# Optimization experiments

Measured on AMD Instinct MI355X. Metric: run time of the kernel, lower is better.

## Reference

```python
import jax, jax.numpy as jnp
import numpy as np

WD = 7                      # width == height == 7 (hard-coded 6/7 constants in source)
SCALE = 0.3
NUM_CLASSES = 17
IN_FEAT = NUM_CLASSES * 10 * WD * WD  # 8330
BS = 4096
GROUPS = [("head", 2), ("arm", 2), ("upper", 2), ("lower", 2), ("foot", 1)]
KEY_IDX = {"head": [0, 1, 3, 4], "arm": [7, 8, 9, 10], "upper": [5, 6, 11, 12],
           "lower": [11, 12, 13, 14], "foot": [15, 16]}


def setup_inputs() -> dict:
    key = jax.random.key(0)
    ks = jax.random.split(key, 2 + 2 * len(GROUPS))
    inp = {
        "x": jax.random.normal(ks[0], (BS, IN_FEAT), jnp.float32),
        "keypoint": jax.random.uniform(ks[1], (BS, 17, 2), jnp.float32),
    }
    i = 2
    for name, g in GROUPS:
        inp[f"W_{name}"] = jax.random.normal(ks[i], (IN_FEAT, g * 2 * WD), jnp.float32) * 0.01
        inp[f"b_{name}"] = jax.random.normal(ks[i + 1], (g * 2 * WD,), jnp.float32) * 0.01
        i += 2
    return inp


def _gen_map(vec, kp):
    """vec: (bs, G, 2, WD) float; kp: (bs, K, 2) int32. Returns (bs, G, 1, WD, WD)."""
    v = jnp.exp(jax.nn.softmax(vec, axis=2))  # softmax over the size-2 axis, then exp
    cols = jnp.arange(WD)

    def cum(a, keep):  # masked normalize + cumsum; a: (bs,G,WD), keep: (bs,1,WD) bool
        am = jnp.where(keep, a, 0.0)
        return jnp.cumsum(am / am.sum(-1, keepdims=True), axis=-1)

    def axis_mask(a, k):  # a: (bs,G,WD), k: (bs,K) int
        lo = jnp.maximum(k.min(axis=1) - 1, 0)[:, None, None]          # zero cols < lo
        hi = jnp.minimum(k.max(axis=1) + 1, WD - 1)[:, None, None]      # zero cols >= hi
        c1 = cum(a, cols >= lo)
        c1 = jnp.where(c1 >= SCALE, c1, 0.0)
        c2 = 1.0 - cum(a, cols < hi)
        c2 = jnp.where(c2 >= SCALE, c2, 0.0)
        return c1 * c2

    xm = axis_mask(v[:, :, 0], kp[:, :, 0])   # (bs,G,WD)
    ym = axis_mask(v[:, :, 1], kp[:, :, 1])   # (bs,G,WD)
    m = ym[:, :, :, None] * xm[:, :, None, :]  # (bs,G,WD,WD): rows=y, cols=x
    # per-sample global max over (G,WD,WD); .item() in torch detaches it
    mx = jax.lax.stop_gradient(m.max(axis=(1, 2, 3), keepdims=True))
    m = m / (mx + 1e-7)
    return m[:, :, None]  # (bs, G, 1, WD, WD)


def reference(x, keypoint, W_head, b_head, W_arm, b_arm, W_upper, b_upper,
              W_lower, b_lower, W_foot, b_foot):
    bs = x.shape[0]
    kp = jnp.minimum(jnp.floor(keypoint * 7.0).astype(jnp.int32), 6)  # (bs,17,2)
    params = {"head": (W_head, b_head), "arm": (W_arm, b_arm),
              "upper": (W_upper, b_upper), "lower": (W_lower, b_lower),
              "foot": (W_foot, b_foot)}
    outs = []
    for name, _ in GROUPS:
        W, b = params[name]
        vec = (x @ W + b).reshape(bs, -1, 2, WD)            # (bs,G,2,WD)
        outs.append(_gen_map(vec, kp[:, jnp.array(KEY_IDX[name])]))
    return tuple(outs)
```

## Files before the change

### kernel.cpp

```cpp
#include <hip/hip_runtime.h>

typedef _Float16 half8 __attribute__((ext_vector_type(8)));
typedef float f32x4 __attribute__((ext_vector_type(4)));

#define WD 7
#define NPAD 128
#define KDIM 8330
#define BSZ 4096
#define SPLITK 8
#define NTILES 261
#define BM 64
#define BK 32

static constexpr size_t OFF_WT   = 0;
static constexpr size_t WT_BYTES = (size_t)NTILES * 16384;
static constexpr size_t OFF_BIAS = WT_BYTES;
static constexpr size_t OFF_PART = OFF_BIAS + 512;

static __device__ const int KIDX[5][4] = {
    {0, 1, 3, 4}, {7, 8, 9, 10}, {5, 6, 11, 12}, {11, 12, 13, 14}, {15, 16, 15, 16}};
static __device__ const unsigned long long OBASE[5] = {0ull, 401408ull, 802816ull, 1204224ull, 1605632ull};

__device__ __forceinline__ int tile0_of(int s) { return 33 * s - max(0, s - 5); }
__device__ __forceinline__ int niter_of(int s) { return (s < 5) ? 33 : 32; }

__device__ __forceinline__ unsigned pk16(_Float16 a, _Float16 b) {
  return (unsigned)__builtin_bit_cast(unsigned short, a) |
         ((unsigned)__builtin_bit_cast(unsigned short, b) << 16);
}

__device__ __forceinline__ void gload_lds4(const void* g, void* l) {
  __builtin_amdgcn_global_load_lds((const __attribute__((address_space(1))) unsigned int*)g,
                                   (__attribute__((address_space(3))) unsigned int*)l, 4, 0, 0);
}
__device__ __forceinline__ void gload_lds16(const void* g, void* l) {
  __builtin_amdgcn_global_load_lds((const __attribute__((address_space(1))) unsigned int*)g,
                                   (__attribute__((address_space(3))) unsigned int*)l, 16, 0, 0);
}

__global__ __launch_bounds__(256) void pack_kernel(
    const float* __restrict__ Wh, const float* __restrict__ bh,
    const float* __restrict__ Wa, const float* __restrict__ ba,
    const float* __restrict__ Wu, const float* __restrict__ bu,
    const float* __restrict__ Wl_, const float* __restrict__ bl,
    const float* __restrict__ Wf, const float* __restrict__ bf,
    char* __restrict__ wsb) {
  _Float16* wt = (_Float16*)(wsb + OFF_WT);
  float* bias = (float*)(wsb + OFF_BIAS);
  __shared__ _Float16 sh[64][128];
  __shared__ _Float16 sl[64][128];
  const int k0 = blockIdx.x * 64;
  const int tid = threadIdx.x;

#pragma unroll
  for (int jj = 0; jj < 32; ++jj) {
    int idx = tid + 256 * jj;
    int kk = idx >> 7, n = idx & 127;
    int k = k0 + kk;
    float w = 0.f;
    if (k < KDIM) {
      if      (n < 28)  w = Wh [k * 28 + n];
      else if (n < 56)  w = Wa [k * 28 + (n - 28)];
      else if (n < 84)  w = Wu [k * 28 + (n - 56)];
      else if (n < 112) w = Wl_[k * 28 + (n - 84)];
      else if (n < 126) w = Wf [k * 14 + (n - 112)];
    }
    _Float16 h = (_Float16)w;
    _Float16 l = (_Float16)((w - (float)h) * 2048.0f);
    sh[kk][n] = h;
    sl[kk][n] = l;
  }
  if (blockIdx.x == 0 && tid < NPAD) {
    int n = tid;
    float v = 0.f;
    if      (n < 28)  v = bh[n];
    else if (n < 56)  v = ba[n - 28];
    else if (n < 84)  v = bu[n - 56];
    else if (n < 112) v = bl[n - 84];
    else if (n < 126) v = bf[n - 112];
    bias[n] = v;
  }
  __syncthreads();
  const int n = tid >> 1;
  const int kc = (tid & 1) * 32;
  const int kglob = k0 + kc;
  if (kglob < NTILES * 32) {
    const int tile = kglob >> 5;
    _Float16* tb = wt + (size_t)tile * 8192;
#pragma unroll
    for (int c = 0; c < 4; ++c) {
      int sp = c ^ ((n >> 1) & 3);
      uint4 qh, ql;
      qh.x = pk16(sh[kc + c * 8 + 0][n], sh[kc + c * 8 + 1][n]);
      qh.y = pk16(sh[kc + c * 8 + 2][n], sh[kc + c * 8 + 3][n]);
      qh.z = pk16(sh[kc + c * 8 + 4][n], sh[kc + c * 8 + 5][n]);
      qh.w = pk16(sh[kc + c * 8 + 6][n], sh[kc + c * 8 + 7][n]);
      ql.x = pk16(sl[kc + c * 8 + 0][n], sl[kc + c * 8 + 1][n]);
      ql.y = pk16(sl[kc + c * 8 + 2][n], sl[kc + c * 8 + 3][n]);
      ql.z = pk16(sl[kc + c * 8 + 4][n], sl[kc + c * 8 + 5][n]);
      ql.w = pk16(sl[kc + c * 8 + 6][n], sl[kc + c * 8 + 7][n]);
      *(uint4*)(tb + (size_t)n * 32 + sp * 8)        = qh;
      *(uint4*)(tb + 4096 + (size_t)n * 32 + sp * 8) = ql;
    }
  }
}

__global__ __launch_bounds__(256) void gemm_kernel(const float* __restrict__ x,
                                                   char* __restrict__ wsb) {
  const _Float16* wt = (const _Float16*)(wsb + OFF_WT);
  float* partial = (float*)(wsb + OFF_PART);
  const int bid = blockIdx.x;
  const int split = bid & 7;
  const int row0 = (bid >> 3) * BM;
  const int tile0 = tile0_of(split);
  const int ks = tile0 * 32;
  const int niter = niter_of(split);

  __shared__ float alds[3][64][32];
  __shared__ _Float16 wlds[2][128][32];

  const int tid = threadIdx.x;
  const int lane = tid & 63;
  const int wid = tid >> 6;
  const int wm = wid & 1;
  const int wn = wid >> 1;

  const int rowlane = lane >> 5;
  const int up = (lane >> 2) & 7;
  const int fof = lane & 3;
  const float* xsrc[8];
#pragma unroll
  for (int j = 0; j < 8; ++j) {
    int row = wid * 16 + 2 * j + rowlane;
    int koff = ((up ^ (row & 7)) << 2) + fof;
    xsrc[j] = x + (size_t)(row0 + row) * KDIM + koff;
  }
  auto stageX = [&](int buf, int kb) {
    if (kb + BK <= KDIM) {
#pragma unroll
      for (int j = 0; j < 8; ++j)
        gload_lds4((const void*)(xsrc[j] + kb), (void*)&alds[buf][wid * 16 + 2 * j][0]);
    } else {
#pragma unroll
      for (int j = 0; j < 8; ++j) {
        int row = wid * 16 + 2 * j + rowlane;
        int k = kb + ((up ^ (row & 7)) << 2) + fof;
        float v = (k < KDIM) ? x[(size_t)(row0 + row) * KDIM + k] : 0.f;
        alds[buf][row][lane & 31] = v;
      }
    }
  };

  auto stageW = [&](int tile) {
    const _Float16* src = wt + (size_t)tile * 8192 + (size_t)wid * 2048 + (size_t)lane * 8;
#pragma unroll
    for (int c = 0; c < 4; ++c) {
      int chunk = wid * 4 + c;
      gload_lds16((const void*)(src + c * 512),
                  (void*)((char*)&wlds[0][0][0] + chunk * 1024));
    }
  };

  f32x4 accA[2][4], accB[2][4];
#pragma unroll
  for (int mt = 0; mt < 2; ++mt)
#pragma unroll
    for (int nt = 0; nt < 4; ++nt) { accA[mt][nt] = (f32x4)(0.f); accB[mt][nt] = (f32x4)(0.f); }

  const int fr = lane & 15;
  const int fslot = lane >> 4;

  stageW(tile0);
  stageX(0, ks);
  stageX(1, ks + BK);
  asm volatile("s_waitcnt vmcnt(8) lgkmcnt(0)" ::: "memory");
  __builtin_amdgcn_s_barrier();

  int xbuf = 0;
  for (int t = 0; t < niter; ++t) {
    float4 fa[2], fb[2];
    half8 b_h[4], b_l[4];
#pragma unroll
    for (int mt = 0; mt < 2; ++mt) {
      int row = wm * 32 + mt * 16 + fr;
      int u0 = (2 * fslot) ^ (row & 7);
      int u1 = (2 * fslot + 1) ^ (row & 7);
      fa[mt] = *(const float4*)&alds[xbuf][row][u0 * 4];
      fb[mt] = *(const float4*)&alds[xbuf][row][u1 * 4];
    }
#pragma unroll
    for (int nt = 0; nt < 4; ++nt) {
      int col = wn * 64 + nt * 16 + fr;
      int sp = fslot ^ ((col >> 1) & 3);
      b_h[nt] = *(const half8*)&wlds[0][col][sp * 8];
      b_l[nt] = *(const half8*)&wlds[1][col][sp * 8];
    }
    asm volatile("s_waitcnt lgkmcnt(0)" ::: "memory");
    __builtin_amdgcn_s_barrier();

    if (t + 1 < niter) stageW(tile0 + t + 1);
    if (t + 2 < niter) {
      int nb = xbuf + 2; if (nb >= 3) nb -= 3;
      stageX(nb, ks + (t + 2) * BK);
    }
    __builtin_amdgcn_sched_barrier(0);

    half8 a_h[2], a_l[2];
#pragma unroll
    for (int mt = 0; mt < 2; ++mt) {
      float fv[8] = {fa[mt].x, fa[mt].y, fa[mt].z, fa[mt].w,
                     fb[mt].x, fb[mt].y, fb[mt].z, fb[mt].w};
#pragma unroll
      for (int i = 0; i < 8; ++i) {
        _Float16 h = (_Float16)fv[i];
        a_h[mt][i] = h;
        a_l[mt][i] = (_Float16)((fv[i] - (float)h) * 2048.0f);
      }
    }
    __builtin_amdgcn_s_setprio(1);
#pragma unroll
    for (int mt = 0; mt < 2; ++mt)
#pragma unroll
      for (int nt = 0; nt < 4; ++nt) {
        accA[mt][nt] = __builtin_amdgcn_mfma_f32_16x16x32_f16(a_h[mt], b_h[nt], accA[mt][nt], 0, 0, 0);
        accB[mt][nt] = __builtin_amdgcn_mfma_f32_16x16x32_f16(a_l[mt], b_h[nt], accB[mt][nt], 0, 0, 0);
        accB[mt][nt] = __builtin_amdgcn_mfma_f32_16x16x32_f16(a_h[mt], b_l[nt], accB[mt][nt], 0, 0, 0);
      }
    __builtin_amdgcn_s_setprio(0);

    if (t + 1 < niter) {
      if (t + 2 < niter)
        asm volatile("s_waitcnt vmcnt(8) lgkmcnt(0)" ::: "memory");
      else
        asm volatile("s_waitcnt vmcnt(0) lgkmcnt(0)" ::: "memory");
      __builtin_amdgcn_s_barrier();
    }
    ++xbuf; if (xbuf >= 3) xbuf = 0;
  }

  float* pb = partial + (size_t)split * BSZ * NPAD;
#pragma unroll
  for (int mt = 0; mt < 2; ++mt)
#pragma unroll
    for (int nt = 0; nt < 4; ++nt) {
      int col = wn * 64 + nt * 16 + fr;
#pragma unroll
      for (int r = 0; r < 4; ++r) {
        int row = row0 + wm * 32 + mt * 16 + fslot * 4 + r;
        pb[(size_t)row * NPAD + col] = accA[mt][nt][r] + accB[mt][nt][r] * (1.0f / 2048.0f);
      }
    }
}

__device__ __forceinline__ void axis_mask(const float a[WD], int lo, int hi, float m[WD]) {
  float am[WD];
  float tot = 0.f;
#pragma unroll
  for (int c = 0; c < WD; ++c) { am[c] = (c >= lo) ? a[c] : 0.f; tot += am[c]; }
  float run = 0.f;
  float c1[WD];
#pragma unroll
  for (int c = 0; c < WD; ++c) {
    run += am[c] / tot;
    c1[c] = (run >= 0.3f) ? run : 0.f;
  }
  float tot2 = 0.f;
#pragma unroll
  for (int c = 0; c < WD; ++c) { am[c] = (c < hi) ? a[c] : 0.f; tot2 += am[c]; }
  run = 0.f;
#pragma unroll
  for (int c = 0; c < WD; ++c) {
    run += am[c] / tot2;
    float c2 = 1.f - run;
    c2 = (c2 >= 0.3f) ? c2 : 0.f;
    m[c] = c1[c] * c2;
  }
}

__global__ __launch_bounds__(256) void epi_kernel(const char* __restrict__ wsb,
                                                  const float* __restrict__ keypoint,
                                                  float* __restrict__ out) {
  __shared__ float vlds[64][132];
  const int b0 = blockIdx.x * 64;
  const int tid = threadIdx.x;
  const float4* part4 = (const float4*)(wsb + OFF_PART);
  const float4* bias4 = (const float4*)(wsb + OFF_BIAS);

  float4 a[8];
#pragma unroll
  for (int j = 0; j < 8; ++j) {
    int fi = tid * 8 + j;
    a[j] = part4[((size_t)(b0 + (fi >> 5))) * 32 + (fi & 31)];
  }
  for (int sp = 1; sp < SPLITK; ++sp) {
#pragma unroll
    for (int j = 0; j < 8; ++j) {
      int fi = tid * 8 + j;
      float4 p = part4[((size_t)sp * BSZ + b0 + (fi >> 5)) * 32 + (fi & 31)];
      a[j].x += p.x; a[j].y += p.y; a[j].z += p.z; a[j].w += p.w;
    }
  }
#pragma unroll
  for (int j = 0; j < 8; ++j) {
    int fi = tid * 8 + j;
    float4 bb = bias4[fi & 31];
    a[j].x += bb.x; a[j].y += bb.y; a[j].z += bb.z; a[j].w += bb.w;
    *(float4*)&vlds[fi >> 5][(fi & 31) * 4] = a[j];
  }
  __syncthreads();

  for (int u = tid; u < 64 * 5; u += 256) {
    int fam = u >> 6;
    int bl = u & 63;
    int b = b0 + bl;
    const int G = (fam == 4) ? 1 : 2;
    const int nk = (fam == 4) ? 2 : 4;
    const float* vv = &vlds[bl][fam * 28];

    int mnx = 7, mxx = -1, mny = 7, mxy = -1;
    for (int i = 0; i < nk; ++i) {
      int kidx = KIDX[fam][i];
      float fx = keypoint[((size_t)b * 17 + kidx) * 2 + 0];
      float fy = keypoint[((size_t)b * 17 + kidx) * 2 + 1];
      int ix = (int)floorf(fx * 7.0f); ix = ix < 6 ? ix : 6;
      int iy = (int)floorf(fy * 7.0f); iy = iy < 6 ? iy : 6;
      mnx = min(mnx, ix); mxx = max(mxx, ix);
      mny = min(mny, iy); mxy = max(mxy, iy);
    }
    int lox = mnx - 1; if (lox < 0) lox = 0;
    int hix = mxx + 1; if (hix > 6) hix = 6;
    int loy = mny - 1; if (loy < 0) loy = 0;
    int hiy = mxy + 1; if (hiy > 6) hiy = 6;

    float xmg[2][WD], ymg[2][WD];
    float mx = 0.f;
#pragma unroll
    for (int g = 0; g < 2; ++g) {
      if (g < G) {
        const float* vg = vv + g * 14;
        float a0[WD], a1[WD];
#pragma unroll
        for (int c = 0; c < WD; ++c) {
          float s0 = vg[c], s1 = vg[c + 7];
          float mM = fmaxf(s0, s1);
          float e0 = expf(s0 - mM), e1 = expf(s1 - mM);
          float sum = e0 + e1;
          a0[c] = expf(e0 / sum);
          a1[c] = expf(e1 / sum);
        }
        axis_mask(a0, lox, hix, xmg[g]);
        axis_mask(a1, loy, hiy, ymg[g]);
        float mx_x = 0.f, mx_y = 0.f;
#pragma unroll
        for (int c = 0; c < WD; ++c) {
          mx_x = fmaxf(mx_x, xmg[g][c]);
          mx_y = fmaxf(mx_y, ymg[g][c]);
        }
        mx = fmaxf(mx, mx_y * mx_x);
      }
    }

    float d = mx + 1e-7f;
    float* op = out + OBASE[fam] + (size_t)b * (G * 49);
#pragma unroll
    for (int g = 0; g < 2; ++g) {
      if (g < G) {
#pragma unroll
        for (int y = 0; y < WD; ++y) {
          float yv = ymg[g][y];
#pragma unroll
          for (int xx = 0; xx < WD; ++xx) {
            op[g * 49 + y * 7 + xx] = (yv * xmg[g][xx]) / d;
          }
        }
      }
    }
  }
}

extern "C" void kernel_launch(void* const* d_in, const int* in_sizes, int n_in,
                              void* d_out, int out_size, void* d_ws, size_t ws_size,
                              hipStream_t stream) {
  const float* x        = (const float*)d_in[0];
  const float* keypoint = (const float*)d_in[1];
  const float* Wh = (const float*)d_in[2];
  const float* bh = (const float*)d_in[3];
  const float* Wa = (const float*)d_in[4];
  const float* ba = (const float*)d_in[5];
  const float* Wu = (const float*)d_in[6];
  const float* bu = (const float*)d_in[7];
  const float* Wl = (const float*)d_in[8];
  const float* bl = (const float*)d_in[9];
  const float* Wf = (const float*)d_in[10];
  const float* bf = (const float*)d_in[11];
  float* out = (float*)d_out;
  char* wsb  = (char*)d_ws;

  const int packBlocks = (NTILES * 32 + 63) / 64;
  hipLaunchKernelGGL(pack_kernel, dim3(packBlocks), dim3(256), 0, stream,
                     Wh, bh, Wa, ba, Wu, bu, Wl, bl, Wf, bf, wsb);
  hipLaunchKernelGGL(gemm_kernel, dim3((BSZ / BM) * SPLITK), dim3(256), 0, stream, x, wsb);
  hipLaunchKernelGGL(epi_kernel, dim3(BSZ / 64), dim3(256), 0, stream,
                     wsb, keypoint, out);
}
```

Before: 85.72 us.

## Double the GEMM K-tile to 64 with reworked swizzle and packing

Raises the K step per pipeline iteration from 32 to 64, so each iteration stages twice as much x and packed-weight data and runs two MFMA sub-steps per barrier. The weight pack layout, the LDS swizzles for x and W, the split-K tile assignment and the vmcnt wait counts all change to match, and LDS moves to a dynamic allocation of about 80 KB. The aim is to halve barriers and loop overhead per unit of K. The larger LDS footprint and higher register pressure may reduce occupancy.

```diff
diff --git a/kernel.cpp b/kernel.cpp
--- a/kernel.cpp
+++ b/kernel.cpp
@@ -8,21 +8,24 @@
 #define KDIM 8330
 #define BSZ 4096
 #define SPLITK 8
-#define NTILES 261
+#define NTILES 131
 #define BM 64
-#define BK 32
+#define BK 64
 
 static constexpr size_t OFF_WT   = 0;
-static constexpr size_t WT_BYTES = (size_t)NTILES * 16384;
+static constexpr size_t WT_BYTES = (size_t)NTILES * 32768;
 static constexpr size_t OFF_BIAS = WT_BYTES;
 static constexpr size_t OFF_PART = OFF_BIAS + 512;
+
+#define LDS_X_BYTES (3 * 64 * 64 * 4)
+#define LDS_TOTAL   (LDS_X_BYTES + 32768)
 
 static __device__ const int KIDX[5][4] = {
     {0, 1, 3, 4}, {7, 8, 9, 10}, {5, 6, 11, 12}, {11, 12, 13, 14}, {15, 16, 15, 16}};
 static __device__ const unsigned long long OBASE[5] = {0ull, 401408ull, 802816ull, 1204224ull, 1605632ull};
 
-__device__ __forceinline__ int tile0_of(int s) { return 33 * s - max(0, s - 5); }
-__device__ __forceinline__ int niter_of(int s) { return (s < 5) ? 33 : 32; }
+__device__ __forceinline__ int tile0_of(int s) { return 16 * s + min(s, 3); }
+__device__ __forceinline__ int niter_of(int s) { return (s < 3) ? 17 : 16; }
 
 __device__ __forceinline__ unsigned pk16(_Float16 a, _Float16 b) {
   return (unsigned)__builtin_bit_cast(unsigned short, a) |
@@ -49,7 +52,8 @@
   float* bias = (float*)(wsb + OFF_BIAS);
   __shared__ _Float16 sh[64][128];
   __shared__ _Float16 sl[64][128];
-  const int k0 = blockIdx.x * 64;
+  const int tile = blockIdx.x;
+  const int k0 = tile * 64;
   const int tid = threadIdx.x;
 
 #pragma unroll
@@ -82,42 +86,41 @@
   }
   __syncthreads();
   const int n = tid >> 1;
-  const int kc = (tid & 1) * 32;
-  const int kglob = k0 + kc;
-  if (kglob < NTILES * 32) {
-    const int tile = kglob >> 5;
-    _Float16* tb = wt + (size_t)tile * 8192;
-#pragma unroll
-    for (int c = 0; c < 4; ++c) {
-      int sp = c ^ ((n >> 1) & 3);
-      uint4 qh, ql;
-      qh.x = pk16(sh[kc + c * 8 + 0][n], sh[kc + c * 8 + 1][n]);
-      qh.y = pk16(sh[kc + c * 8 + 2][n], sh[kc + c * 8 + 3][n]);
-      qh.z = pk16(sh[kc + c * 8 + 4][n], sh[kc + c * 8 + 5][n]);
-      qh.w = pk16(sh[kc + c * 8 + 6][n], sh[kc + c * 8 + 7][n]);
-      ql.x = pk16(sl[kc + c * 8 + 0][n], sl[kc + c * 8 + 1][n]);
-      ql.y = pk16(sl[kc + c * 8 + 2][n], sl[kc + c * 8 + 3][n]);
-      ql.z = pk16(sl[kc + c * 8 + 4][n], sl[kc + c * 8 + 5][n]);
-      ql.w = pk16(sl[kc + c * 8 + 6][n], sl[kc + c * 8 + 7][n]);
-      *(uint4*)(tb + (size_t)n * 32 + sp * 8)        = qh;
-      *(uint4*)(tb + 4096 + (size_t)n * 32 + sp * 8) = ql;
-    }
+  const int chalf = (tid & 1) * 4;
+  _Float16* tb = wt + (size_t)tile * 16384;
+#pragma unroll
+  for (int c4 = 0; c4 < 4; ++c4) {
+    int c = chalf + c4;
+    int sp = c ^ (n & 7);
+    int kc = c * 8;
+    uint4 qh, ql;
+    qh.x = pk16(sh[kc + 0][n], sh[kc + 1][n]);
+    qh.y = pk16(sh[kc + 2][n], sh[kc + 3][n]);
+    qh.z = pk16(sh[kc + 4][n], sh[kc + 5][n]);
+    qh.w = pk16(sh[kc + 6][n], sh[kc + 7][n]);
+    ql.x = pk16(sl[kc + 0][n], sl[kc + 1][n]);
+    ql.y = pk16(sl[kc + 2][n], sl[kc + 3][n]);
+    ql.z = pk16(sl[kc + 4][n], sl[kc + 5][n]);
+    ql.w = pk16(sl[kc + 6][n], sl[kc + 7][n]);
+    *(uint4*)(tb + (size_t)n * 64 + sp * 8)        = qh;
+    *(uint4*)(tb + 8192 + (size_t)n * 64 + sp * 8) = ql;
   }
 }
 
 __global__ __launch_bounds__(256) void gemm_kernel(const float* __restrict__ x,
                                                    char* __restrict__ wsb) {
+  extern __shared__ char ldsbuf[];
+  float (*alds)[64][64] = (float(*)[64][64])ldsbuf;
+  _Float16* wlds = (_Float16*)(ldsbuf + LDS_X_BYTES);
+
   const _Float16* wt = (const _Float16*)(wsb + OFF_WT);
   float* partial = (float*)(wsb + OFF_PART);
   const int bid = blockIdx.x;
   const int split = bid & 7;
   const int row0 = (bid >> 3) * BM;
   const int tile0 = tile0_of(split);
-  const int ks = tile0 * 32;
+  const int ks = tile0 * 64;
   const int niter = niter_of(split);
-
-  __shared__ float alds[3][64][32];
-  __shared__ _Float16 wlds[2][128][32];
 
   const int tid = threadIdx.x;
   const int lane = tid & 63;
@@ -125,39 +128,38 @@
   const int wm = wid & 1;
   const int wn = wid >> 1;
 
-  const int rowlane = lane >> 5;
-  const int up = (lane >> 2) & 7;
-  const int fof = lane & 3;
-  const float* xsrc[8];
-#pragma unroll
-  for (int j = 0; j < 8; ++j) {
-    int row = wid * 16 + 2 * j + rowlane;
-    int koff = ((up ^ (row & 7)) << 2) + fof;
+  const int u_ln = lane >> 2;
+  const int f_ln = lane & 3;
+  const float* xsrc[16];
+#pragma unroll
+  for (int j = 0; j < 16; ++j) {
+    int row = wid * 16 + j;
+    int koff = ((u_ln ^ (row & 15)) << 2) + f_ln;
     xsrc[j] = x + (size_t)(row0 + row) * KDIM + koff;
   }
   auto stageX = [&](int buf, int kb) {
     if (kb + BK <= KDIM) {
 #pragma unroll
-      for (int j = 0; j < 8; ++j)
-        gload_lds4((const void*)(xsrc[j] + kb), (void*)&alds[buf][wid * 16 + 2 * j][0]);
+      for (int j = 0; j < 16; ++j)
+        gload_lds4((const void*)(xsrc[j] + kb), (void*)&alds[buf][wid * 16 + j][0]);
     } else {
 #pragma unroll
-      for (int j = 0; j < 8; ++j) {
-        int row = wid * 16 + 2 * j + rowlane;
-        int k = kb + ((up ^ (row & 7)) << 2) + fof;
+      for (int j = 0; j < 16; ++j) {
+        int row = wid * 16 + j;
+        int k = kb + ((u_ln ^ (row & 15)) << 2) + f_ln;
         float v = (k < KDIM) ? x[(size_t)(row0 + row) * KDIM + k] : 0.f;
-        alds[buf][row][lane & 31] = v;
+        alds[buf][row][lane] = v;
       }
     }
   };
 
   auto stageW = [&](int tile) {
-    const _Float16* src = wt + (size_t)tile * 8192 + (size_t)wid * 2048 + (size_t)lane * 8;
-#pragma unroll
-    for (int c = 0; c < 4; ++c) {
-      int chunk = wid * 4 + c;
+    const _Float16* src = wt + (size_t)tile * 16384 + (size_t)wid * 4096 + (size_t)lane * 8;
+#pragma unroll
+    for (int c = 0; c < 8; ++c) {
+      int chunk = wid * 8 + c;
       gload_lds16((const void*)(src + c * 512),
-                  (void*)((char*)&wlds[0][0][0] + chunk * 1024));
+                  (void*)((char*)wlds + chunk * 1024));
     }
   };
 
@@ -173,28 +175,32 @@
   stageW(tile0);
   stageX(0, ks);
   stageX(1, ks + BK);
-  asm volatile("s_waitcnt vmcnt(8) lgkmcnt(0)" ::: "memory");
+  asm volatile("s_waitcnt vmcnt(16) lgkmcnt(0)" ::: "memory");
   __builtin_amdgcn_s_barrier();
 
   int xbuf = 0;
   for (int t = 0; t < niter; ++t) {
-    float4 fa[2], fb[2];
-    half8 b_h[4], b_l[4];
-#pragma unroll
-    for (int mt = 0; mt < 2; ++mt) {
-      int row = wm * 32 + mt * 16 + fr;
-      int u0 = (2 * fslot) ^ (row & 7);
-      int u1 = (2 * fslot + 1) ^ (row & 7);
-      fa[mt] = *(const float4*)&alds[xbuf][row][u0 * 4];
-      fb[mt] = *(const float4*)&alds[xbuf][row][u1 * 4];
-    }
-#pragma unroll
-    for (int nt = 0; nt < 4; ++nt) {
-      int col = wn * 64 + nt * 16 + fr;
-      int sp = fslot ^ ((col >> 1) & 3);
-      b_h[nt] = *(const half8*)&wlds[0][col][sp * 8];
-      b_l[nt] = *(const half8*)&wlds[1][col][sp * 8];
-    }
+    float4 fA[2][2], fB[2][2];
+    half8 b_h[2][4], b_l[2][4];
+#pragma unroll
+    for (int ks2 = 0; ks2 < 2; ++ks2)
+#pragma unroll
+      for (int mt = 0; mt < 2; ++mt) {
+        int row = wm * 32 + mt * 16 + fr;
+        int u0 = (ks2 * 8 + 2 * fslot) ^ (row & 15);
+        int u1 = (ks2 * 8 + 2 * fslot + 1) ^ (row & 15);
+        fA[ks2][mt] = *(const float4*)&alds[xbuf][row][u0 * 4];
+        fB[ks2][mt] = *(const float4*)&alds[xbuf][row][u1 * 4];
+      }
+#pragma unroll
+    for (int ks2 = 0; ks2 < 2; ++ks2)
+#pragma unroll
+      for (int nt = 0; nt < 4; ++nt) {
+        int col = wn * 64 + nt * 16 + fr;
+        int sp = (ks2 * 4 + fslot) ^ (col & 7);
+        b_h[ks2][nt] = *(const half8*)(wlds + (size_t)col * 64 + sp * 8);
+        b_l[ks2][nt] = *(const half8*)(wlds + 8192 + (size_t)col * 64 + sp * 8);
+      }
     asm volatile("s_waitcnt lgkmcnt(0)" ::: "memory");
     __builtin_amdgcn_s_barrier();
 
@@ -205,32 +211,35 @@
     }
     __builtin_amdgcn_sched_barrier(0);
 
-    half8 a_h[2], a_l[2];
-#pragma unroll
-    for (int mt = 0; mt < 2; ++mt) {
-      float fv[8] = {fa[mt].x, fa[mt].y, fa[mt].z, fa[mt].w,
-                     fb[mt].x, fb[mt].y, fb[mt].z, fb[mt].w};
-#pragma unroll
-      for (int i = 0; i < 8; ++i) {
-        _Float16 h = (_Float16)fv[i];
-        a_h[mt][i] = h;
-        a_l[mt][i] = (_Float16)((fv[i] - (float)h) * 2048.0f);
-      }
-    }
-    __builtin_amdgcn_s_setprio(1);
-#pragma unroll
-    for (int mt = 0; mt < 2; ++mt)
-#pragma unroll
-      for (int nt = 0; nt < 4; ++nt) {
-        accA[mt][nt] = __builtin_amdgcn_mfma_f32_16x16x32_f16(a_h[mt], b_h[nt], accA[mt][nt], 0, 0, 0);
-        accB[mt][nt] = __builtin_amdgcn_mfma_f32_16x16x32_f16(a_l[mt], b_h[nt], accB[mt][nt], 0, 0, 0);
-        accB[mt][nt] = __builtin_amdgcn_mfma_f32_16x16x32_f16(a_h[mt], b_l[nt], accB[mt][nt], 0, 0, 0);
-      }
-    __builtin_amdgcn_s_setprio(0);
+#pragma unroll
+    for (int ks2 = 0; ks2 < 2; ++ks2) {
+      half8 a_h[2], a_l[2];
+#pragma unroll
+      for (int mt = 0; mt < 2; ++mt) {
+        float fv[8] = {fA[ks2][mt].x, fA[ks2][mt].y, fA[ks2][mt].z, fA[ks2][mt].w,
+                       fB[ks2][mt].x, fB[ks2][mt].y, fB[ks2][mt].z, fB[ks2][mt].w};
+#pragma unroll
+        for (int i = 0; i < 8; ++i) {
+          _Float16 h = (_Float16)fv[i];
+          a_h[mt][i] = h;
+          a_l[mt][i] = (_Float16)((fv[i] - (float)h) * 2048.0f);
+        }
+      }
+      __builtin_amdgcn_s_setprio(1);
+#pragma unroll
+      for (int mt = 0; mt < 2; ++mt)
+#pragma unroll
+        for (int nt = 0; nt < 4; ++nt) {
+          accA[mt][nt] = __builtin_amdgcn_mfma_f32_16x16x32_f16(a_h[mt], b_h[ks2][nt], accA[mt][nt], 0, 0, 0);
+          accB[mt][nt] = __builtin_amdgcn_mfma_f32_16x16x32_f16(a_l[mt], b_h[ks2][nt], accB[mt][nt], 0, 0, 0);
+          accB[mt][nt] = __builtin_amdgcn_mfma_f32_16x16x32_f16(a_h[mt], b_l[ks2][nt], accB[mt][nt], 0, 0, 0);
+        }
+      __builtin_amdgcn_s_setprio(0);
+    }
 
     if (t + 1 < niter) {
       if (t + 2 < niter)
-        asm volatile("s_waitcnt vmcnt(8) lgkmcnt(0)" ::: "memory");
+        asm volatile("s_waitcnt vmcnt(16) lgkmcnt(0)" ::: "memory");
       else
         asm volatile("s_waitcnt vmcnt(0) lgkmcnt(0)" ::: "memory");
       __builtin_amdgcn_s_barrier();
@@ -396,10 +405,13 @@
   float* out = (float*)d_out;
   char* wsb  = (char*)d_ws;
 
-  const int packBlocks = (NTILES * 32 + 63) / 64;
-  hipLaunchKernelGGL(pack_kernel, dim3(packBlocks), dim3(256), 0, stream,
+  (void)hipFuncSetAttribute(reinterpret_cast<const void*>(gemm_kernel),
+                            hipFuncAttributeMaxDynamicSharedMemorySize, LDS_TOTAL);
+
+  hipLaunchKernelGGL(pack_kernel, dim3(NTILES), dim3(256), 0, stream,
                      Wh, bh, Wa, ba, Wu, bu, Wl, bl, Wf, bf, wsb);
-  hipLaunchKernelGGL(gemm_kernel, dim3((BSZ / BM) * SPLITK), dim3(256), 0, stream, x, wsb);
+  hipLaunchKernelGGL(gemm_kernel, dim3((BSZ / BM) * SPLITK), dim3(256), LDS_TOTAL, stream,
+                     x, wsb);
   hipLaunchKernelGGL(epi_kernel, dim3(BSZ / 64), dim3(256), 0, stream,
                      wsb, keypoint, out);
 }
```

Result: slower. 99.13 us (+15.6%).
